# Optimization experiments

Hardware: AMD Instinct MI355X
Metric: run time of the kernel (lower is better)

## Reference

```python
import jax, jax.numpy as jnp
import numpy as np

N = 1024   # num_nodes
M = 1152   # max_node_number
L = 32     # tree depth (NATree.shape[1])
K = M - N + 1  # Conv2 kernel size = 129


def setup_inputs() -> dict:
    key = jax.random.key(0)
    ks = jax.random.split(key, 6)
    NATree = jax.random.normal(ks[0], (N, L, M), jnp.float32)
    # self.x ~ U(-1/sqrt(M), 1/sqrt(M)) per reset_parameters
    stdv = 1.0 / np.sqrt(M)
    x = jax.random.uniform(ks[1], (N, M), jnp.float32, -stdv, stdv)
    # Conv1d(in=M, out=M, k=2): torch default init U(-s, s), s = 1/sqrt(in*k)
    cs = 1.0 / np.sqrt(M * 2)
    convW = jax.random.uniform(ks[2], (M, M, 2), jnp.float32, -cs, cs)
    convb = jax.random.uniform(ks[3], (M,), jnp.float32, -cs, cs)
    # Conv1d(in=1, out=1, k=K)
    c2s = 1.0 / np.sqrt(K)
    conv2W = jax.random.uniform(ks[4], (1, 1, K), jnp.float32, -c2s, c2s)
    conv2b = jax.random.uniform(ks[5], (1,), jnp.float32, -c2s, c2s)
    return dict(NATree=NATree, x=x, convW=convW, convb=convb,
                conv2W=conv2W, conv2b=conv2b)


def reference(NATree, x, convW, convb, conv2W, conv2b):
    # Conv1d(in=M,out=M,k=2) on [1,M,2] is out[o] = sum_m W[o,m,0]*r[m] + W[o,m,1]*h[m] + b[o]
    W0 = convW[:, :, 0]  # [M, M] acts on the current row
    W1 = convW[:, :, 1]  # [M, M] acts on the running state
    h0 = NATree[:, -1, :]                                   # [N, M]
    rows = jnp.flip(NATree[:, :-1, :], axis=1)              # j = L-2 .. 0
    rows = rows.transpose(1, 0, 2)                          # [L-1, N, M]

    def step(h, r):
        h_new = jnp.tanh(r @ W0.T + h @ W1.T + convb) + r   # [N, M]
        return h_new, None

    h, _ = jax.lax.scan(step, h0, rows)                     # [N, M]
    total = jnp.tanh(h)
    res = jnp.tanh(total + x)                               # [N, M]
    # Conv2: input permuted to [N, 1, M], 1->1 channels, kernel K -> [N, 1, N]
    out = jax.lax.conv_general_dilated(
        res[:, None, :], conv2W, window_strides=(1,), padding='VALID',
        dimension_numbers=('NCH', 'OIH', 'NCH'))
    out = out + conv2b[None, :, None]
    return out[:, 0, :]                                     # [N, N]
```

## Files before the change

kernel.cpp:

```cpp
#include <hip/hip_runtime.h>
#include <hip/hip_bf16.h>

#define N_ 1024
#define M_ 1152
#define L_ 32
#define NATSTRIDE (L_*M_)
#define CONVK 129
#define OUTW 1024
#define NSTEP 31

typedef __attribute__((ext_vector_type(8))) short short8;
typedef __attribute__((ext_vector_type(4))) float f32x4;

__device__ __forceinline__ unsigned short f2bf(float f) {
    unsigned int u = __float_as_uint(f);
    u += 0x7FFFu + ((u >> 16) & 1u);
    return (unsigned short)(u >> 16);
}
__device__ __forceinline__ float bf2f(unsigned short b) {
    return __uint_as_float(((unsigned int)b) << 16);
}

__global__ __launch_bounds__(256) void build_wsplit(const float* __restrict__ convW,
                                                    unsigned short* __restrict__ w0t,
                                                    unsigned short* __restrict__ w1t) {
    int idx = blockIdx.x * blockDim.x + threadIdx.x;
    if (idx >= M_ * M_) return;
    int m = idx / M_;
    int k = idx - m * M_;
    const float* s = convW + (size_t)m * (2 * M_) + 2 * k;
    w0t[idx] = f2bf(s[0]);
    w1t[idx] = f2bf(s[1]);
}

__global__ __launch_bounds__(256) void build_h0(const float* __restrict__ nat,
                                                unsigned short* __restrict__ hblk) {
    int idx = blockIdx.x * blockDim.x + threadIdx.x;
    if (idx >= N_ * M_ / 8) return;
    int n = idx / (M_ / 8);
    int c = idx - n * (M_ / 8);
    const float* s = nat + (size_t)n * NATSTRIDE + (size_t)(L_ - 1) * M_ + c * 8;
    f32x4 v0 = *(const f32x4*)(s);
    f32x4 v1 = *(const f32x4*)(s + 4);
    short8 tt;
    #pragma unroll
    for (int e = 0; e < 4; ++e) {
        tt[e]     = (short)f2bf(v0[e]);
        tt[4 + e] = (short)f2bf(v1[e]);
    }
    *(short8*)(hblk + (size_t)c * 8192 + (size_t)n * 8) = tt;
}

__global__ __launch_bounds__(256) void build_rbf(const float* __restrict__ nat,
                                                 unsigned short* __restrict__ rbf) {
    int idx = blockIdx.x * blockDim.x + threadIdx.x;
    if (idx >= NSTEP * N_ * M_ / 8) return;
    int o = idx * 8;
    int t = o / (N_ * M_);
    int rem = o - t * (N_ * M_);
    int n = rem / M_;
    int m = rem - n * M_;
    int l = (NSTEP - 1) - t;
    const float* s = nat + (size_t)n * NATSTRIDE + (size_t)l * M_ + m;
    f32x4 v0 = *(const f32x4*)(s);
    f32x4 v1 = *(const f32x4*)(s + 4);
    short8 tt;
    #pragma unroll
    for (int e = 0; e < 4; ++e) {
        tt[e]     = (short)f2bf(v0[e]);
        tt[4 + e] = (short)f2bf(v1[e]);
    }
    *(short8*)(rbf + o) = tt;
}

#define P_BM 128
#define P_BN 128
#define P_BK 64
#define P_NT (M_ / P_BK)
#define P_LDP 72

__global__ __launch_bounds__(256) void rpre_gemm(
    const unsigned short* __restrict__ rbf,
    const unsigned short* __restrict__ w0t,
    const float* __restrict__ convb,
    unsigned short* __restrict__ rpre)
{
    __shared__ __align__(16) unsigned short As[2][P_BM * P_LDP];
    __shared__ __align__(16) unsigned short Bs[2][P_BN * P_LDP];

    int tid = threadIdx.x;
    int lane = tid & 63;
    int w = tid >> 6;
    int wr = w >> 1, wc = w & 1;
    int raw = blockIdx.y * 9 + blockIdx.x;
    int logical = (raw & 7) * 279 + (raw >> 3);
    int bx = logical % 9, by = logical / 9;
    int n0 = by * P_BM;
    int m0 = bx * P_BN;

    int lr = lane & 15;
    int lk = (lane >> 4) * 8;
    int srow = tid >> 3;
    int skcol = (tid & 7) * 8;

    f32x4 acc[4][4] = {};

    auto loadTile = [&](int it, short8 a[4], short8 b[4]) {
        int kb = it * P_BK;
        #pragma unroll
        for (int i = 0; i < 4; ++i) {
            int row = srow + i * 32;
            a[i] = *(const short8*)(rbf + (size_t)(n0 + row) * M_ + kb + skcol);
            b[i] = *(const short8*)(w0t + (size_t)(m0 + row) * M_ + kb + skcol);
        }
    };
    auto writeTile = [&](int buf, short8 a[4], short8 b[4]) {
        #pragma unroll
        for (int i = 0; i < 4; ++i) {
            *(short8*)&As[buf][(srow + i * 32) * P_LDP + skcol] = a[i];
            *(short8*)&Bs[buf][(srow + i * 32) * P_LDP + skcol] = b[i];
        }
    };

    {
        short8 a0[4], b0[4];
        loadTile(0, a0, b0);
        writeTile(0, a0, b0);
    }
    __syncthreads();

    int cur = 0;
    for (int it = 0; it < P_NT; ++it) {
        short8 a2[4], b2[4];
        if (it + 1 < P_NT) loadTile(it + 1, a2, b2);

        #pragma unroll
        for (int ks = 0; ks < P_BK; ks += 32) {
            short8 af[4], bf_[4];
            #pragma unroll
            for (int mi = 0; mi < 4; ++mi)
                af[mi] = *(const short8*)&As[cur][(wr * 64 + mi * 16 + lr) * P_LDP + ks + lk];
            #pragma unroll
            for (int ni = 0; ni < 4; ++ni)
                bf_[ni] = *(const short8*)&Bs[cur][(wc * 64 + ni * 16 + lr) * P_LDP + ks + lk];
            #pragma unroll
            for (int mi = 0; mi < 4; ++mi)
                #pragma unroll
                for (int ni = 0; ni < 4; ++ni)
                    acc[mi][ni] = __builtin_amdgcn_mfma_f32_16x16x32_bf16(
                        af[mi], bf_[ni], acc[mi][ni], 0, 0, 0);
        }
        if (it + 1 < P_NT) {
            writeTile(cur ^ 1, a2, b2);
            __syncthreads();
            cur ^= 1;
        }
    }

    #pragma unroll
    for (int mi = 0; mi < 4; ++mi) {
        #pragma unroll
        for (int ni = 0; ni < 4; ++ni) {
            int mloc = m0 + wc * 64 + ni * 16 + lr;
            float bias = convb[mloc];
            #pragma unroll
            for (int j = 0; j < 4; ++j) {
                int g = n0 + wr * 64 + mi * 16 + (lane >> 4) * 4 + j;
                rpre[(size_t)g * M_ + mloc] = f2bf(acc[mi][ni][j] + bias);
            }
        }
    }
}

#define PS_LDP 1160

__global__ __launch_bounds__(256) void panel_step(
    const unsigned short* __restrict__ hin,
    const unsigned short* __restrict__ w1t,
    const unsigned short* __restrict__ rpre_t,
    const unsigned short* __restrict__ rbf_t,
    const float* __restrict__ x,
    unsigned short* __restrict__ hout,
    float* __restrict__ resOut,
    int final_step)
{
    __shared__ __align__(16) unsigned short Bs[64 * PS_LDP];

    int tid = threadIdx.x;
    int lane = tid & 63;
    int w = tid >> 6;
    int bid = blockIdx.x;
    int rg = bid & 7;
    int cg = bid >> 3;
    int n0 = rg * 128;
    int m0 = cg * 64;
    int lr = lane & 15;
    int lg = lane >> 4;

    {
        int col = tid >> 2;
        int q = tid & 3;
        const unsigned short* src = w1t + (size_t)(m0 + col) * M_;
        unsigned short* dst = &Bs[col * PS_LDP];
        #pragma unroll
        for (int j = 0; j < 36; ++j) {
            int e = (q + 4 * j) * 8;
            *(short8*)(dst + e) = *(const short8*)(src + e);
        }
    }

    int R0 = n0 + 32 * w + lr;
    int R1 = R0 + 16;
    const unsigned short* hb0 = hin + (size_t)R0 * 8;
    const unsigned short* hb1 = hin + (size_t)R1 * 8;
    short8 aQ[6][2];
    auto loadA = [&](int it) {
        int s = it % 6;
        size_t co = (size_t)(it * 4 + lg) * 8192;
        aQ[s][0] = *(const short8*)(hb0 + co);
        aQ[s][1] = *(const short8*)(hb1 + co);
    };
    loadA(0); loadA(1); loadA(2); loadA(3); loadA(4); loadA(5);

    unsigned short preR[2][4][4], rbfR[2][4][4];
    #pragma unroll
    for (int mi = 0; mi < 2; ++mi)
        #pragma unroll
        for (int ni = 0; ni < 4; ++ni) {
            int mloc = m0 + ni * 16 + lr;
            #pragma unroll
            for (int j = 0; j < 4; ++j) {
                int nloc = n0 + 32 * w + 16 * mi + lg * 4 + j;
                preR[mi][ni][j] = rpre_t[(size_t)nloc * M_ + mloc];
                rbfR[mi][ni][j] = rbf_t[(size_t)nloc * M_ + mloc];
            }
        }

    __syncthreads();

    f32x4 acc[2][4] = {};
    #pragma unroll
    for (int it = 0; it < 36; ++it) {
        short8 bf_[4];
        #pragma unroll
        for (int ni = 0; ni < 4; ++ni)
            bf_[ni] = *(const short8*)&Bs[(ni * 16 + lr) * PS_LDP + it * 32 + lg * 8];
        int s = it % 6;
        #pragma unroll
        for (int ni = 0; ni < 4; ++ni) {
            acc[0][ni] = __builtin_amdgcn_mfma_f32_16x16x32_bf16(aQ[s][0], bf_[ni], acc[0][ni], 0, 0, 0);
            acc[1][ni] = __builtin_amdgcn_mfma_f32_16x16x32_bf16(aQ[s][1], bf_[ni], acc[1][ni], 0, 0, 0);
        }
        if (it + 6 < 36) loadA(it + 6);
    }

    #pragma unroll
    for (int mi = 0; mi < 2; ++mi) {
        #pragma unroll
        for (int ni = 0; ni < 4; ++ni) {
            int mloc = m0 + ni * 16 + lr;
            int cB = mloc >> 3, eB = mloc & 7;
            #pragma unroll
            for (int j = 0; j < 4; ++j) {
                int nloc = n0 + 32 * w + 16 * mi + lg * 4 + j;
                float pre = acc[mi][ni][j] + bf2f(preR[mi][ni][j]);
                float hv = tanhf(pre) + bf2f(rbfR[mi][ni][j]);
                if (final_step) {
                    resOut[(size_t)nloc * M_ + mloc] = tanhf(tanhf(hv) + x[(size_t)nloc * M_ + mloc]);
                } else {
                    hout[(size_t)cB * 8192 + (size_t)nloc * 8 + eB] = f2bf(hv);
                }
            }
        }
    }
}

__global__ __launch_bounds__(256) void conv_out_kernel(
    const float* __restrict__ res, const float* __restrict__ w2,
    const float* __restrict__ b2, float* __restrict__ out)
{
    __shared__ float row[M_];
    __shared__ float wk[CONVK];
    int n = blockIdx.x;
    int tid = threadIdx.x;
    for (int i = tid; i < M_; i += 256) row[i] = res[(size_t)n * M_ + i];
    if (tid < CONVK) wk[tid] = w2[tid];
    __syncthreads();
    float b = b2[0];
    int j0 = tid * 4;
    float s0 = b, s1 = b, s2 = b, s3 = b;
    float r0 = row[j0], r1 = row[j0 + 1], r2 = row[j0 + 2], r3 = row[j0 + 3];
    for (int k = 0; k < CONVK; ++k) {
        float wv = wk[k];
        s0 += r0 * wv; s1 += r1 * wv; s2 += r2 * wv; s3 += r3 * wv;
        if (k < CONVK - 1) { r0 = r1; r1 = r2; r2 = r3; r3 = row[j0 + 4 + k]; }
    }
    float* o = out + (size_t)n * OUTW + j0;
    o[0] = s0; o[1] = s1; o[2] = s2; o[3] = s3;
}

extern "C" void kernel_launch(void* const* d_in, const int* in_sizes, int n_in,
                              void* d_out, int out_size, void* d_ws, size_t ws_size,
                              hipStream_t stream) {
    const float* NATree = (const float*)d_in[0];
    const float* x      = (const float*)d_in[1];
    const float* convW  = (const float*)d_in[2];
    const float* convb  = (const float*)d_in[3];
    const float* conv2W = (const float*)d_in[4];
    const float* conv2b = (const float*)d_in[5];
    float* out = (float*)d_out;

    char* ws = (char*)d_ws;
    size_t off = 0;
    auto alloc = [&](size_t bytes) {
        void* p = ws + off;
        off = (off + bytes + 255) & ~(size_t)255;
        return p;
    };
    unsigned short* w0t  = (unsigned short*)alloc((size_t)M_ * M_ * 2);
    unsigned short* w1t  = (unsigned short*)alloc((size_t)M_ * M_ * 2);
    unsigned short* hA   = (unsigned short*)alloc((size_t)N_ * M_ * 2);
    unsigned short* hB   = (unsigned short*)alloc((size_t)N_ * M_ * 2);
    unsigned short* rpre = (unsigned short*)alloc((size_t)NSTEP * N_ * M_ * 2);
    unsigned short* rbf  = (unsigned short*)alloc((size_t)NSTEP * N_ * M_ * 2);
    float*          res  = (float*)alloc((size_t)N_ * M_ * 4);

    build_wsplit<<<(M_ * M_ + 255) / 256, 256, 0, stream>>>(convW, w0t, w1t);
    build_h0<<<(N_ * M_ / 8 + 255) / 256, 256, 0, stream>>>(NATree, hA);
    build_rbf<<<(NSTEP * N_ * M_ / 8 + 255) / 256, 256, 0, stream>>>(NATree, rbf);

    rpre_gemm<<<dim3(M_ / P_BN, (NSTEP * N_) / P_BM), 256, 0, stream>>>(rbf, w0t, convb, rpre);

    const unsigned short* hin = hA;
    unsigned short* hout = hB;
    for (int t = 0; t < NSTEP; ++t) {
        int fin = (t == NSTEP - 1) ? 1 : 0;
        panel_step<<<144, 256, 0, stream>>>(
            hin, w1t, rpre + (size_t)t * N_ * M_, rbf + (size_t)t * N_ * M_,
            x, hout, res, fin);
        unsigned short* tmp = hout;
        hout = (unsigned short*)hin;
        hin = tmp;
    }

    conv_out_kernel<<<1024, 256, 0, stream>>>(res, conv2W, conv2b, out);
}
```

Before: 646.6 us.

## Drop LDS staging in recurrent step; load blocked W1 directly into registers

W1 is now stored in a k-blocked layout (8-element chunks per row) so each lane can fetch MFMA B fragments straight from global memory, the same way the hidden-state A fragments are fetched. The per-step kernel no longer copies a 64x1152 panel of W1 into LDS and no longer needs the block barrier. Each block covers 32 output columns instead of 64, so the grid doubles to 288 blocks. The tradeoff is that W1 is fetched from global/L2 by more blocks, and each block does fewer MFMAs per A load, which lowers reuse.

Result: faster. 585.1 us (-9.5%).

```diff
diff --git a/kernel.cpp b/kernel.cpp
--- a/kernel.cpp
+++ b/kernel.cpp
@@ -23,14 +23,15 @@
 
 __global__ __launch_bounds__(256) void build_wsplit(const float* __restrict__ convW,
                                                     unsigned short* __restrict__ w0t,
-                                                    unsigned short* __restrict__ w1t) {
+                                                    unsigned short* __restrict__ w1blk) {
     int idx = blockIdx.x * blockDim.x + threadIdx.x;
     if (idx >= M_ * M_) return;
     int m = idx / M_;
     int k = idx - m * M_;
     const float* s = convW + (size_t)m * (2 * M_) + 2 * k;
     w0t[idx] = f2bf(s[0]);
-    w1t[idx] = f2bf(s[1]);
+    int c = k >> 3, e = k & 7;
+    w1blk[(size_t)c * 9216 + (size_t)m * 8 + e] = f2bf(s[1]);
 }
 
 __global__ __launch_bounds__(256) void build_h0(const float* __restrict__ nat,
@@ -172,11 +173,9 @@
     }
 }
 
-#define PS_LDP 1160
-
-__global__ __launch_bounds__(256) void panel_step(
+__global__ __launch_bounds__(256) void nolds_step(
     const unsigned short* __restrict__ hin,
-    const unsigned short* __restrict__ w1t,
+    const unsigned short* __restrict__ w1blk,
     const unsigned short* __restrict__ rpre_t,
     const unsigned short* __restrict__ rbf_t,
     const float* __restrict__ x,
@@ -184,8 +183,6 @@
     float* __restrict__ resOut,
     int final_step)
 {
-    __shared__ __align__(16) unsigned short Bs[64 * PS_LDP];
-
     int tid = threadIdx.x;
     int lane = tid & 63;
     int w = tid >> 6;
@@ -193,40 +190,33 @@
     int rg = bid & 7;
     int cg = bid >> 3;
     int n0 = rg * 128;
-    int m0 = cg * 64;
+    int m0 = cg * 32;
     int lr = lane & 15;
     int lg = lane >> 4;
 
-    {
-        int col = tid >> 2;
-        int q = tid & 3;
-        const unsigned short* src = w1t + (size_t)(m0 + col) * M_;
-        unsigned short* dst = &Bs[col * PS_LDP];
-        #pragma unroll
-        for (int j = 0; j < 36; ++j) {
-            int e = (q + 4 * j) * 8;
-            *(short8*)(dst + e) = *(const short8*)(src + e);
-        }
-    }
-
     int R0 = n0 + 32 * w + lr;
-    int R1 = R0 + 16;
     const unsigned short* hb0 = hin + (size_t)R0 * 8;
-    const unsigned short* hb1 = hin + (size_t)R1 * 8;
-    short8 aQ[6][2];
-    auto loadA = [&](int it) {
-        int s = it % 6;
-        size_t co = (size_t)(it * 4 + lg) * 8192;
-        aQ[s][0] = *(const short8*)(hb0 + co);
-        aQ[s][1] = *(const short8*)(hb1 + co);
+    const unsigned short* hb1 = hb0 + 16 * 8;
+    const unsigned short* wb0 = w1blk + (size_t)(m0 + lr) * 8;
+    const unsigned short* wb1 = wb0 + 16 * 8;
+
+    short8 aQ[4][2], bQ[4][2];
+    auto loadQ = [&](int it) {
+        int s = it & 3;
+        size_t ca = (size_t)(it * 4 + lg) * 8192;
+        size_t cb = (size_t)(it * 4 + lg) * 9216;
+        aQ[s][0] = *(const short8*)(hb0 + ca);
+        aQ[s][1] = *(const short8*)(hb1 + ca);
+        bQ[s][0] = *(const short8*)(wb0 + cb);
+        bQ[s][1] = *(const short8*)(wb1 + cb);
     };
-    loadA(0); loadA(1); loadA(2); loadA(3); loadA(4); loadA(5);
-
-    unsigned short preR[2][4][4], rbfR[2][4][4];
+    loadQ(0); loadQ(1); loadQ(2); loadQ(3);
+
+    unsigned short preR[2][2][4], rbfR[2][2][4];
     #pragma unroll
     for (int mi = 0; mi < 2; ++mi)
         #pragma unroll
-        for (int ni = 0; ni < 4; ++ni) {
+        for (int ni = 0; ni < 2; ++ni) {
             int mloc = m0 + ni * 16 + lr;
             #pragma unroll
             for (int j = 0; j < 4; ++j) {
@@ -236,28 +226,23 @@
             }
         }
 
-    __syncthreads();
-
-    f32x4 acc[2][4] = {};
+    f32x4 acc[2][2] = {};
     #pragma unroll
     for (int it = 0; it < 36; ++it) {
-        short8 bf_[4];
-        #pragma unroll
-        for (int ni = 0; ni < 4; ++ni)
-            bf_[ni] = *(const short8*)&Bs[(ni * 16 + lr) * PS_LDP + it * 32 + lg * 8];
-        int s = it % 6;
-        #pragma unroll
-        for (int ni = 0; ni < 4; ++ni) {
-            acc[0][ni] = __builtin_amdgcn_mfma_f32_16x16x32_bf16(aQ[s][0], bf_[ni], acc[0][ni], 0, 0, 0);
-            acc[1][ni] = __builtin_amdgcn_mfma_f32_16x16x32_bf16(aQ[s][1], bf_[ni], acc[1][ni], 0, 0, 0);
-        }
-        if (it + 6 < 36) loadA(it + 6);
+        int s = it & 3;
+        #pragma unroll
+        for (int mi = 0; mi < 2; ++mi)
+            #pragma unroll
+            for (int ni = 0; ni < 2; ++ni)
+                acc[mi][ni] = __builtin_amdgcn_mfma_f32_16x16x32_bf16(
+                    aQ[s][mi], bQ[s][ni], acc[mi][ni], 0, 0, 0);
+        if (it + 4 < 36) loadQ(it + 4);
     }
 
     #pragma unroll
     for (int mi = 0; mi < 2; ++mi) {
         #pragma unroll
-        for (int ni = 0; ni < 4; ++ni) {
+        for (int ni = 0; ni < 2; ++ni) {
             int mloc = m0 + ni * 16 + lr;
             int cB = mloc >> 3, eB = mloc & 7;
             #pragma unroll
@@ -317,15 +302,15 @@
         off = (off + bytes + 255) & ~(size_t)255;
         return p;
     };
-    unsigned short* w0t  = (unsigned short*)alloc((size_t)M_ * M_ * 2);
-    unsigned short* w1t  = (unsigned short*)alloc((size_t)M_ * M_ * 2);
-    unsigned short* hA   = (unsigned short*)alloc((size_t)N_ * M_ * 2);
-    unsigned short* hB   = (unsigned short*)alloc((size_t)N_ * M_ * 2);
-    unsigned short* rpre = (unsigned short*)alloc((size_t)NSTEP * N_ * M_ * 2);
-    unsigned short* rbf  = (unsigned short*)alloc((size_t)NSTEP * N_ * M_ * 2);
-    float*          res  = (float*)alloc((size_t)N_ * M_ * 4);
-
-    build_wsplit<<<(M_ * M_ + 255) / 256, 256, 0, stream>>>(convW, w0t, w1t);
+    unsigned short* w0t   = (unsigned short*)alloc((size_t)M_ * M_ * 2);
+    unsigned short* w1blk = (unsigned short*)alloc((size_t)M_ * M_ * 2);
+    unsigned short* hA    = (unsigned short*)alloc((size_t)N_ * M_ * 2);
+    unsigned short* hB    = (unsigned short*)alloc((size_t)N_ * M_ * 2);
+    unsigned short* rpre  = (unsigned short*)alloc((size_t)NSTEP * N_ * M_ * 2);
+    unsigned short* rbf   = (unsigned short*)alloc((size_t)NSTEP * N_ * M_ * 2);
+    float*          res   = (float*)alloc((size_t)N_ * M_ * 4);
+
+    build_wsplit<<<(M_ * M_ + 255) / 256, 256, 0, stream>>>(convW, w0t, w1blk);
     build_h0<<<(N_ * M_ / 8 + 255) / 256, 256, 0, stream>>>(NATree, hA);
     build_rbf<<<(NSTEP * N_ * M_ / 8 + 255) / 256, 256, 0, stream>>>(NATree, rbf);
 
@@ -335,8 +320,8 @@
     unsigned short* hout = hB;
     for (int t = 0; t < NSTEP; ++t) {
         int fin = (t == NSTEP - 1) ? 1 : 0;
-        panel_step<<<144, 256, 0, stream>>>(
-            hin, w1t, rpre + (size_t)t * N_ * M_, rbf + (size_t)t * N_ * M_,
+        nolds_step<<<288, 256, 0, stream>>>(
+            hin, w1blk, rpre + (size_t)t * N_ * M_, rbf + (size_t)t * N_ * M_,
             x, hout, res, fin);
         unsigned short* tmp = hout;
         hout = (unsigned short*)hin;
```
